# Kernel optimization log

Measured on AMD Instinct MI355X. Metric: run time of the kernel, lower is better.

The kernel has to match this reference:

```python
import jax, jax.numpy as jnp
import numpy as np

SOFTCAP = 30.0


def setup_inputs() -> dict:
    key = jax.random.key(0)
    ks = jax.random.split(key, 5)
    T, H, E, I = 2048, 2048, 8, 4096
    scale_h = 1.0 / np.sqrt(H)
    scale_i = 1.0 / np.sqrt(I)
    return {
        "hidden_states": jax.random.normal(ks[0], (T, H), dtype=jnp.float32),
        "gate_w": jax.random.normal(ks[1], (H, E), dtype=jnp.float32) * scale_h,
        "w_gate": jax.random.normal(ks[2], (E, H, I), dtype=jnp.float32) * scale_h,
        "w_up": jax.random.normal(ks[3], (E, H, I), dtype=jnp.float32) * scale_h,
        "w_down": jax.random.normal(ks[4], (E, I, H), dtype=jnp.float32) * scale_i,
        "top_k": 2,
    }


def _route(hidden_states, gate_w, top_k):
    # Router: fp32 gate linear + tanh softcap + global softmax, then top-k select
    logits = jnp.dot(hidden_states.astype(jnp.float32), gate_w)  # [T, E]
    logits = jnp.tanh(logits / SOFTCAP) * SOFTCAP
    probs = jax.nn.softmax(logits, axis=-1)  # softmax over ALL experts
    _, topk_idx = jax.lax.top_k(logits, top_k)  # [T, k], indices from raw logits
    topk_w = jnp.take_along_axis(probs, topk_idx, axis=-1)  # no renormalize
    return topk_w, topk_idx


def reference(hidden_states, gate_w, w_gate, w_up, w_down, top_k):
    T, H = hidden_states.shape
    E = gate_w.shape[-1]
    topk_w, topk_idx = _route(hidden_states, gate_w, top_k)
    # Combine weights: scatter top-k weights into dense [T, E] (indices distinct)
    combine = jnp.zeros((T, E), dtype=hidden_states.dtype)
    combine = combine.at[jnp.arange(T)[:, None], topk_idx].set(
        topk_w.astype(hidden_states.dtype))
    # Expert gated-GELU MLP, dense dispatch (reference semantics of EPMoE)
    g = jnp.einsum("th,ehi->eti", hidden_states, w_gate)  # [E, T, I]
    u = jnp.einsum("th,ehi->eti", hidden_states, w_up)
    act = jax.nn.gelu(g) * u
    out_e = jnp.einsum("eti,eih->eth", act, w_down)  # [E, T, H]
    out = jnp.einsum("eth,te->th", out_e, combine)  # weighted combine
    return out
```

## Files before the change

### kernel.cpp

```cpp
#include <hip/hip_runtime.h>
#include <stdint.h>

typedef unsigned short u16;
typedef short short8 __attribute__((ext_vector_type(8)));
typedef short short4v __attribute__((ext_vector_type(4)));
typedef float f32x4 __attribute__((ext_vector_type(4)));

#define T_TOK 2048
#define H_DIM 2048
#define E_NUM 8
#define I_DIM 4096
#define BM 256
#define MAXTILES 24

__device__ __forceinline__ u16 f2bf(float f) {
    union { float f; uint32_t u; } v; v.f = f;
    uint32_t u = v.u;
    u += 0x7fffu + ((u >> 16) & 1u);
    return (u16)(u >> 16);
}

__device__ __forceinline__ float gelu_tanh(float x) {
    float t = tanhf(0.7978845608028654f * (x + 0.044715f * x * x * x));
    return 0.5f * x * (1.0f + t);
}

__global__ void router_kernel(const float* __restrict__ hid, const float* __restrict__ gw,
                              u16* __restrict__ xbf, int* __restrict__ tidx,
                              float* __restrict__ tw, int* __restrict__ cnt) {
    int tid = threadIdx.x;
    int wv = tid >> 6, lane = tid & 63;
    int t = blockIdx.x * 4 + wv;
    const float* xrow = hid + (size_t)t * H_DIM;
    float acc[8];
#pragma unroll
    for (int e = 0; e < 8; e++) acc[e] = 0.f;
    for (int h0 = 0; h0 < H_DIM; h0 += 64) {
        float x = xrow[h0 + lane];
        xbf[(size_t)t * H_DIM + h0 + lane] = f2bf(x);
        const float4* g4 = (const float4*)(gw + (size_t)(h0 + lane) * 8);
        float4 ga = g4[0], gb = g4[1];
        acc[0] += x * ga.x; acc[1] += x * ga.y; acc[2] += x * ga.z; acc[3] += x * ga.w;
        acc[4] += x * gb.x; acc[5] += x * gb.y; acc[6] += x * gb.z; acc[7] += x * gb.w;
    }
#pragma unroll
    for (int off = 32; off > 0; off >>= 1) {
#pragma unroll
        for (int e = 0; e < 8; e++) acc[e] += __shfl_down(acc[e], off);
    }
    if (lane == 0) {
        float l[8], p[8];
        float mx = -1e30f;
#pragma unroll
        for (int e = 0; e < 8; e++) { l[e] = 30.0f * tanhf(acc[e] * (1.0f / 30.0f)); mx = fmaxf(mx, l[e]); }
        float s = 0.f;
#pragma unroll
        for (int e = 0; e < 8; e++) { p[e] = expf(l[e] - mx); s += p[e]; }
        int i1 = 0;
#pragma unroll
        for (int e = 1; e < 8; e++) if (l[e] > l[i1]) i1 = e;
        int i2 = (i1 == 0) ? 1 : 0;
#pragma unroll
        for (int e = 0; e < 8; e++) if (e != i1 && l[e] > l[i2]) i2 = e;
        float inv = 1.0f / s;
        tidx[2 * t] = i1;     tw[2 * t] = p[i1] * inv;
        tidx[2 * t + 1] = i2; tw[2 * t + 1] = p[i2] * inv;
        atomicAdd(&cnt[i1], 1);
        atomicAdd(&cnt[i2], 1);
    }
}

__global__ void scan_kernel(const int* __restrict__ cnt, int* seg, int* cur,
                            int* tE, int* tM0, int* tEnd) {
    if (threadIdx.x != 0) return;
    int off = 0, nt = 0;
    for (int e = 0; e < 8; e++) {
        seg[e] = off; cur[e] = off;
        int c = cnt[e];
        for (int m = 0; m < c; m += BM) { tE[nt] = e; tM0[nt] = off + m; tEnd[nt] = off + c; nt++; }
        off += c;
    }
    seg[8] = off;
    for (; nt < MAXTILES; nt++) tE[nt] = -1;
}

__global__ void scatter_kernel(const int* __restrict__ tidx, const float* __restrict__ tw,
                               int* __restrict__ cur, int* __restrict__ ptok,
                               float* __restrict__ pwt) {
    int t = blockIdx.x * blockDim.x + threadIdx.x;
    if (t >= T_TOK) return;
#pragma unroll
    for (int k = 0; k < 2; k++) {
        int e = tidx[2 * t + k];
        int pos = atomicAdd(&cur[e], 1);
        ptok[pos] = t;
        pwt[pos] = tw[2 * t + k];
    }
}

__global__ __launch_bounds__(512, 2)
void gemm1_kernel(const u16* __restrict__ xbf, const float* __restrict__ wg_all,
                  const float* __restrict__ wu_all, u16* __restrict__ Aact,
                  const int* __restrict__ tE, const int* __restrict__ tM0,
                  const int* __restrict__ tEnd, const int* __restrict__ ptok) {
    int e = tE[blockIdx.x];
    if (e < 0) return;
    int m0 = tM0[blockIdx.x], mend = tEnd[blockIdx.x];
    int n0 = blockIdx.y * 128;
    __shared__ __align__(16) u16 As[256 * 40];
    __shared__ __align__(16) u16 Bgs[128 * 40];
    __shared__ __align__(16) u16 Bus[128 * 40];
    __shared__ int ltok[256];
    int tid = threadIdx.x;
    if (tid < 256) { int p = m0 + tid; ltok[tid] = (p < mend) ? ptok[p] : ptok[m0]; }
    __syncthreads();

    int ar0 = tid >> 2, ac = (tid & 3) * 8;
    int ar1 = (tid + 512) >> 2;
    const u16* arow0 = xbf + (size_t)ltok[ar0] * H_DIM;
    const u16* arow1 = xbf + (size_t)ltok[ar1] * H_DIM;
    int half = tid >> 8, tt = tid & 255;
    int bn = (tt & 63) * 2, bk = (tt >> 6) * 8;
    const float* bsrc = (half ? wu_all : wg_all) + (size_t)e * H_DIM * I_DIM + n0 + bn;
    u16* bdst = half ? Bus : Bgs;

    int wv = tid >> 6, lane = tid & 63, q = lane >> 4, ln = lane & 15;
    int wm = (wv & 3) * 64, wn = (wv >> 2) * 64;
    const f32x4 z4 = {0.f, 0.f, 0.f, 0.f};
    f32x4 accG[4][4], accU[4][4];
#pragma unroll
    for (int mi = 0; mi < 4; mi++)
#pragma unroll
        for (int ni = 0; ni < 4; ni++) { accG[mi][ni] = z4; accU[mi][ni] = z4; }

    for (int k0 = 0; k0 < H_DIM; k0 += 32) {
        *(uint4*)&As[ar0 * 40 + ac] = *(const uint4*)(arow0 + k0 + ac);
        *(uint4*)&As[ar1 * 40 + ac] = *(const uint4*)(arow1 + k0 + ac);
        const float* bp = bsrc + (size_t)(k0 + bk) * I_DIM;
        float2 v[8];
#pragma unroll
        for (int j = 0; j < 8; j++) v[j] = *(const float2*)(bp + (size_t)j * I_DIM);
        short8 r0, r1;
#pragma unroll
        for (int j = 0; j < 8; j++) { r0[j] = (short)f2bf(v[j].x); r1[j] = (short)f2bf(v[j].y); }
        *(short8*)&bdst[bn * 40 + bk] = r0;
        *(short8*)&bdst[(bn + 1) * 40 + bk] = r1;
        __syncthreads();

        short8 af[4], bg[4], bu[4];
#pragma unroll
        for (int mi = 0; mi < 4; mi++) af[mi] = *(const short8*)&As[(wm + mi * 16 + ln) * 40 + q * 8];
#pragma unroll
        for (int ni = 0; ni < 4; ni++) {
            bg[ni] = *(const short8*)&Bgs[(wn + ni * 16 + ln) * 40 + q * 8];
            bu[ni] = *(const short8*)&Bus[(wn + ni * 16 + ln) * 40 + q * 8];
        }
#pragma unroll
        for (int mi = 0; mi < 4; mi++)
#pragma unroll
            for (int ni = 0; ni < 4; ni++) {
                accG[mi][ni] = __builtin_amdgcn_mfma_f32_16x16x32_bf16(af[mi], bg[ni], accG[mi][ni], 0, 0, 0);
                accU[mi][ni] = __builtin_amdgcn_mfma_f32_16x16x32_bf16(af[mi], bu[ni], accU[mi][ni], 0, 0, 0);
            }
        __syncthreads();
    }
#pragma unroll
    for (int mi = 0; mi < 4; mi++) {
        int pb = m0 + wm + mi * 16 + q * 4;
#pragma unroll
        for (int r = 0; r < 4; r++) {
            int p = pb + r;
            if (p < mend) {
                u16* orow = Aact + (size_t)p * I_DIM + n0 + wn;
#pragma unroll
                for (int ni = 0; ni < 4; ni++) {
                    float g = accG[mi][ni][r], u = accU[mi][ni][r];
                    orow[ni * 16 + ln] = f2bf(gelu_tanh(g) * u);
                }
            }
        }
    }
}

__global__ __launch_bounds__(1024, 4)
void gemm2_kernel(const u16* __restrict__ Aact, const float* __restrict__ wd_all,
                  float* __restrict__ out, const int* __restrict__ tE,
                  const int* __restrict__ tM0, const int* __restrict__ tEnd,
                  const int* __restrict__ ptok, const float* __restrict__ pwt) {
    int e = tE[blockIdx.x];
    if (e < 0) return;
    int m0 = tM0[blockIdx.x], mend = tEnd[blockIdx.x];
    int n0 = blockIdx.y * 128;
    __shared__ __align__(16) u16 As[256 * 40];
    __shared__ __align__(16) u16 Bs[128 * 40];
    __shared__ int ltok[256];
    __shared__ float lwt[256];
    int tid = threadIdx.x;
    if (tid < 256) {
        int p = m0 + tid; bool vld = p < mend;
        ltok[tid] = vld ? ptok[p] : 0;
        lwt[tid] = vld ? pwt[p] : 0.f;
    }
    int ar = tid >> 2, ac = (tid & 3) * 8;
    const u16* asrc = Aact + (size_t)(m0 + ar) * I_DIM + ac;
    int bn = tid & 127, kq = (tid >> 7) * 4;
    const float* bsrc = wd_all + (size_t)e * I_DIM * H_DIM + (size_t)kq * H_DIM + n0 + bn;
    int wv = tid >> 6, lane = tid & 63, q = lane >> 4, ln = lane & 15;
    int wm = (wv & 3) * 64, wn = (wv >> 2) * 32;
    const f32x4 z4 = {0.f, 0.f, 0.f, 0.f};
    f32x4 acc[4][2];
#pragma unroll
    for (int mi = 0; mi < 4; mi++) { acc[mi][0] = z4; acc[mi][1] = z4; }
    __syncthreads();

    for (int k0 = 0; k0 < I_DIM; k0 += 32) {
        *(uint4*)&As[ar * 40 + ac] = *(const uint4*)(asrc + k0);
        const float* bp = bsrc + (size_t)k0 * H_DIM;
        short4v bv;
#pragma unroll
        for (int j = 0; j < 4; j++) bv[j] = (short)f2bf(bp[(size_t)j * H_DIM]);
        *(short4v*)&Bs[bn * 40 + kq] = bv;
        __syncthreads();

        short8 af[4], bf2[2];
#pragma unroll
        for (int mi = 0; mi < 4; mi++) af[mi] = *(const short8*)&As[(wm + mi * 16 + ln) * 40 + q * 8];
#pragma unroll
        for (int ni = 0; ni < 2; ni++) bf2[ni] = *(const short8*)&Bs[(wn + ni * 16 + ln) * 40 + q * 8];
#pragma unroll
        for (int mi = 0; mi < 4; mi++)
#pragma unroll
            for (int ni = 0; ni < 2; ni++)
                acc[mi][ni] = __builtin_amdgcn_mfma_f32_16x16x32_bf16(af[mi], bf2[ni], acc[mi][ni], 0, 0, 0);
        __syncthreads();
    }
#pragma unroll
    for (int mi = 0; mi < 4; mi++)
#pragma unroll
        for (int r = 0; r < 4; r++) {
            int rl = wm + mi * 16 + q * 4 + r;
            int p = m0 + rl;
            if (p < mend) {
                int tok = ltok[rl];
                float w = lwt[rl];
                float* ob = out + (size_t)tok * H_DIM + n0 + wn;
#pragma unroll
                for (int ni = 0; ni < 2; ni++)
                    atomicAdd(ob + ni * 16 + ln, acc[mi][ni][r] * w);
            }
        }
}

extern "C" void kernel_launch(void* const* d_in, const int* in_sizes, int n_in,
                              void* d_out, int out_size, void* d_ws, size_t ws_size,
                              hipStream_t stream) {
    (void)in_sizes; (void)n_in; (void)out_size; (void)ws_size;
    const float* hid = (const float*)d_in[0];
    const float* gw  = (const float*)d_in[1];
    const float* wg  = (const float*)d_in[2];
    const float* wu  = (const float*)d_in[3];
    const float* wd  = (const float*)d_in[4];
    float* out = (float*)d_out;

    char* ws = (char*)d_ws;
    size_t off = 0;
    u16* xbf  = (u16*)(ws + off); off += (size_t)T_TOK * H_DIM * 2;
    u16* Aact = (u16*)(ws + off); off += (size_t)(2 * T_TOK + BM) * I_DIM * 2;
    int*   ptok = (int*)(ws + off);   off += 2 * T_TOK * 4;
    float* pwt  = (float*)(ws + off); off += 2 * T_TOK * 4;
    int*   tidx = (int*)(ws + off);   off += 2 * T_TOK * 4;
    float* tw   = (float*)(ws + off); off += 2 * T_TOK * 4;
    int* cnt  = (int*)(ws + off); off += 64;
    int* cur  = (int*)(ws + off); off += 64;
    int* seg  = (int*)(ws + off); off += 64;
    int* tE   = (int*)(ws + off); off += 128;
    int* tM0  = (int*)(ws + off); off += 128;
    int* tEnd = (int*)(ws + off); off += 128;

    hipMemsetAsync(cnt, 0, 64, stream);
    hipMemsetAsync(d_out, 0, (size_t)T_TOK * H_DIM * 4, stream);
    router_kernel<<<T_TOK / 4, 256, 0, stream>>>(hid, gw, xbf, tidx, tw, cnt);
    scan_kernel<<<1, 1, 0, stream>>>(cnt, seg, cur, tE, tM0, tEnd);
    scatter_kernel<<<T_TOK / 256, 256, 0, stream>>>(tidx, tw, cur, ptok, pwt);
    gemm1_kernel<<<dim3(MAXTILES, I_DIM / 128), 512, 0, stream>>>(xbf, wg, wu, Aact, tE, tM0, tEnd, ptok);
    gemm2_kernel<<<dim3(MAXTILES, H_DIM / 128), 1024, 0, stream>>>(Aact, wd, out, tE, tM0, tEnd, ptok, pwt);
}
```

Baseline: 1.250 ms.

## Prefetch next K-slice into registers in both MoE GEMMs and retile gemm2

Both expert GEMMs now load the next K-slice of activations and weights into registers while the current slice is stored to LDS and consumed. The goal is to hide global-load latency behind MFMA work. The thread-to-element load mapping is reorganised: each thread covers one row and 16 contiguous columns of A, and one weight column over 16 or 8 k values. gemm2 drops from 1024 to 512 threads, and each wave now computes a 64x64 tile instead of 64x32, which raises register pressure. GELU's tanhf is replaced by an exp-based tanh, which may differ slightly in accuracy.

```diff
diff --git a/kernel.cpp b/kernel.cpp
--- a/kernel.cpp
+++ b/kernel.cpp
@@ -3,7 +3,6 @@
 
 typedef unsigned short u16;
 typedef short short8 __attribute__((ext_vector_type(8)));
-typedef short short4v __attribute__((ext_vector_type(4)));
 typedef float f32x4 __attribute__((ext_vector_type(4)));
 
 #define T_TOK 2048
@@ -21,8 +20,12 @@
 }
 
 __device__ __forceinline__ float gelu_tanh(float x) {
-    float t = tanhf(0.7978845608028654f * (x + 0.044715f * x * x * x));
-    return 0.5f * x * (1.0f + t);
+    float z = 0.7978845608028654f * (x + 0.044715f * x * x * x);
+    float a = fabsf(z);
+    float em = __expf(-2.0f * a);
+    float th = (1.0f - em) / (1.0f + em);
+    th = copysignf(th, z);
+    return 0.5f * x * (1.0f + th);
 }
 
 __global__ void router_kernel(const float* __restrict__ hid, const float* __restrict__ gw,
@@ -115,14 +118,15 @@
     if (tid < 256) { int p = m0 + tid; ltok[tid] = (p < mend) ? ptok[p] : ptok[m0]; }
     __syncthreads();
 
-    int ar0 = tid >> 2, ac = (tid & 3) * 8;
-    int ar1 = (tid + 512) >> 2;
-    const u16* arow0 = xbf + (size_t)ltok[ar0] * H_DIM;
-    const u16* arow1 = xbf + (size_t)ltok[ar1] * H_DIM;
+    int arow = tid & 255;
+    int acol = (tid >> 8) * 16;
+    const u16* aptr = xbf + (size_t)ltok[arow] * H_DIM + acol;
+    u16* asd = &As[arow * 40 + acol];
     int half = tid >> 8, tt = tid & 255;
-    int bn = (tt & 63) * 2, bk = (tt >> 6) * 8;
-    const float* bsrc = (half ? wu_all : wg_all) + (size_t)e * H_DIM * I_DIM + n0 + bn;
-    u16* bdst = half ? Bus : Bgs;
+    int bn = tt & 127;
+    int bkh = (tt >> 7) * 16;
+    const float* bptr = (half ? wu_all : wg_all) + (size_t)e * H_DIM * I_DIM + n0 + bn;
+    u16* bsd = (half ? Bus : Bgs) + bn * 40 + bkh;
 
     int wv = tid >> 6, lane = tid & 63, q = lane >> 4, ln = lane & 15;
     int wm = (wv & 3) * 64, wn = (wv >> 2) * 64;
@@ -133,18 +137,27 @@
 #pragma unroll
         for (int ni = 0; ni < 4; ni++) { accG[mi][ni] = z4; accU[mi][ni] = z4; }
 
+    uint4 pa0 = *(const uint4*)(aptr);
+    uint4 pa1 = *(const uint4*)(aptr + 8);
+    float pb[16];
+#pragma unroll
+    for (int j = 0; j < 16; j++) pb[j] = bptr[(size_t)(bkh + j) * I_DIM];
+
     for (int k0 = 0; k0 < H_DIM; k0 += 32) {
-        *(uint4*)&As[ar0 * 40 + ac] = *(const uint4*)(arow0 + k0 + ac);
-        *(uint4*)&As[ar1 * 40 + ac] = *(const uint4*)(arow1 + k0 + ac);
-        const float* bp = bsrc + (size_t)(k0 + bk) * I_DIM;
-        float2 v[8];
-#pragma unroll
-        for (int j = 0; j < 8; j++) v[j] = *(const float2*)(bp + (size_t)j * I_DIM);
+        *(uint4*)asd = pa0;
+        *(uint4*)(asd + 8) = pa1;
         short8 r0, r1;
 #pragma unroll
-        for (int j = 0; j < 8; j++) { r0[j] = (short)f2bf(v[j].x); r1[j] = (short)f2bf(v[j].y); }
-        *(short8*)&bdst[bn * 40 + bk] = r0;
-        *(short8*)&bdst[(bn + 1) * 40 + bk] = r1;
+        for (int j = 0; j < 8; j++) { r0[j] = (short)f2bf(pb[j]); r1[j] = (short)f2bf(pb[8 + j]); }
+        *(short8*)bsd = r0;
+        *(short8*)(bsd + 8) = r1;
+        if (k0 + 32 < H_DIM) {
+            pa0 = *(const uint4*)(aptr + k0 + 32);
+            pa1 = *(const uint4*)(aptr + k0 + 32 + 8);
+            const float* bp2 = bptr + (size_t)(k0 + 32 + bkh) * I_DIM;
+#pragma unroll
+            for (int j = 0; j < 16; j++) pb[j] = bp2[(size_t)j * I_DIM];
+        }
         __syncthreads();
 
         short8 af[4], bg[4], bu[4];
@@ -166,10 +179,10 @@
     }
 #pragma unroll
     for (int mi = 0; mi < 4; mi++) {
-        int pb = m0 + wm + mi * 16 + q * 4;
+        int pb2 = m0 + wm + mi * 16 + q * 4;
 #pragma unroll
         for (int r = 0; r < 4; r++) {
-            int p = pb + r;
+            int p = pb2 + r;
             if (p < mend) {
                 u16* orow = Aact + (size_t)p * I_DIM + n0 + wn;
 #pragma unroll
@@ -182,7 +195,7 @@
     }
 }
 
-__global__ __launch_bounds__(1024, 4)
+__global__ __launch_bounds__(512, 2)
 void gemm2_kernel(const u16* __restrict__ Aact, const float* __restrict__ wd_all,
                   float* __restrict__ out, const int* __restrict__ tE,
                   const int* __restrict__ tM0, const int* __restrict__ tEnd,
@@ -201,37 +214,57 @@
         ltok[tid] = vld ? ptok[p] : 0;
         lwt[tid] = vld ? pwt[p] : 0.f;
     }
-    int ar = tid >> 2, ac = (tid & 3) * 8;
-    const u16* asrc = Aact + (size_t)(m0 + ar) * I_DIM + ac;
-    int bn = tid & 127, kq = (tid >> 7) * 4;
-    const float* bsrc = wd_all + (size_t)e * I_DIM * H_DIM + (size_t)kq * H_DIM + n0 + bn;
+    int arow = tid & 255;
+    int acol = (tid >> 8) * 16;
+    const u16* aptr = Aact + (size_t)(m0 + arow) * I_DIM + acol;
+    u16* asd = &As[arow * 40 + acol];
+    int bn = tid & 127;
+    int bkh = (tid >> 7) * 8;
+    const float* bptr = wd_all + (size_t)e * I_DIM * H_DIM + n0 + bn;
+    u16* bsd = &Bs[bn * 40 + bkh];
+
     int wv = tid >> 6, lane = tid & 63, q = lane >> 4, ln = lane & 15;
-    int wm = (wv & 3) * 64, wn = (wv >> 2) * 32;
+    int wm = (wv & 3) * 64, wn = (wv >> 2) * 64;
     const f32x4 z4 = {0.f, 0.f, 0.f, 0.f};
-    f32x4 acc[4][2];
-#pragma unroll
-    for (int mi = 0; mi < 4; mi++) { acc[mi][0] = z4; acc[mi][1] = z4; }
+    f32x4 acc[4][4];
+#pragma unroll
+    for (int mi = 0; mi < 4; mi++)
+#pragma unroll
+        for (int ni = 0; ni < 4; ni++) acc[mi][ni] = z4;
+
+    uint4 pa0 = *(const uint4*)(aptr);
+    uint4 pa1 = *(const uint4*)(aptr + 8);
+    float pb[8];
+#pragma unroll
+    for (int j = 0; j < 8; j++) pb[j] = bptr[(size_t)(bkh + j) * H_DIM];
     __syncthreads();
 
     for (int k0 = 0; k0 < I_DIM; k0 += 32) {
-        *(uint4*)&As[ar * 40 + ac] = *(const uint4*)(asrc + k0);
-        const float* bp = bsrc + (size_t)k0 * H_DIM;
-        short4v bv;
-#pragma unroll
-        for (int j = 0; j < 4; j++) bv[j] = (short)f2bf(bp[(size_t)j * H_DIM]);
-        *(short4v*)&Bs[bn * 40 + kq] = bv;
+        *(uint4*)asd = pa0;
+        *(uint4*)(asd + 8) = pa1;
+        short8 r0;
+#pragma unroll
+        for (int j = 0; j < 8; j++) r0[j] = (short)f2bf(pb[j]);
+        *(short8*)bsd = r0;
+        if (k0 + 32 < I_DIM) {
+            pa0 = *(const uint4*)(aptr + k0 + 32);
+            pa1 = *(const uint4*)(aptr + k0 + 32 + 8);
+            const float* bp2 = bptr + (size_t)(k0 + 32 + bkh) * H_DIM;
+#pragma unroll
+            for (int j = 0; j < 8; j++) pb[j] = bp2[(size_t)j * H_DIM];
+        }
         __syncthreads();
 
-        short8 af[4], bf2[2];
+        short8 af[4], bf4[4];
 #pragma unroll
         for (int mi = 0; mi < 4; mi++) af[mi] = *(const short8*)&As[(wm + mi * 16 + ln) * 40 + q * 8];
 #pragma unroll
-        for (int ni = 0; ni < 2; ni++) bf2[ni] = *(const short8*)&Bs[(wn + ni * 16 + ln) * 40 + q * 8];
+        for (int ni = 0; ni < 4; ni++) bf4[ni] = *(const short8*)&Bs[(wn + ni * 16 + ln) * 40 + q * 8];
 #pragma unroll
         for (int mi = 0; mi < 4; mi++)
 #pragma unroll
-            for (int ni = 0; ni < 2; ni++)
-                acc[mi][ni] = __builtin_amdgcn_mfma_f32_16x16x32_bf16(af[mi], bf2[ni], acc[mi][ni], 0, 0, 0);
+            for (int ni = 0; ni < 4; ni++)
+                acc[mi][ni] = __builtin_amdgcn_mfma_f32_16x16x32_bf16(af[mi], bf4[ni], acc[mi][ni], 0, 0, 0);
         __syncthreads();
     }
 #pragma unroll
@@ -245,7 +278,7 @@
                 float w = lwt[rl];
                 float* ob = out + (size_t)tok * H_DIM + n0 + wn;
 #pragma unroll
-                for (int ni = 0; ni < 2; ni++)
+                for (int ni = 0; ni < 4; ni++)
                     atomicAdd(ob + ni * 16 + ln, acc[mi][ni][r] * w);
             }
         }
@@ -283,5 +316,5 @@
     scan_kernel<<<1, 1, 0, stream>>>(cnt, seg, cur, tE, tM0, tEnd);
     scatter_kernel<<<T_TOK / 256, 256, 0, stream>>>(tidx, tw, cur, ptok, pwt);
     gemm1_kernel<<<dim3(MAXTILES, I_DIM / 128), 512, 0, stream>>>(xbf, wg, wu, Aact, tE, tM0, tEnd, ptok);
-    gemm2_kernel<<<dim3(MAXTILES, H_DIM / 128), 1024, 0, stream>>>(Aact, wd, out, tE, tM0, tEnd, ptok, pwt);
-}
+    gemm2_kernel<<<dim3(MAXTILES, H_DIM / 128), 512, 0, stream>>>(Aact, wd, out, tE, tM0, tEnd, ptok, pwt);
+}
```

Result: faster. 1.208 ms (-3.4%).
